# Kernel optimization log

Hardware: AMD Instinct MI355X
Metric: run time of the kernel (lower is better)

## Reference

```python
import jax, jax.numpy as jnp
import numpy as np

P = 8  # patch size (hardcoded in unfold/fold of the original module)


def conv2d(x, w, b, groups=1):
    # x: (N,C,H,W), w: (O, C//groups, 3, 3), 'SAME' padding = padding=1 for 3x3
    y = jax.lax.conv_general_dilated(
        x, w, window_strides=(1, 1), padding='SAME',
        dimension_numbers=('NCHW', 'OIHW', 'NCHW'),
        feature_group_count=groups)
    return y + b[None, :, None, None]


def unfold8(x):
    # F.unfold(kernel=8, stride=8): (N,C,H,W) -> (N, C*64, L), channel-major then
    # kernel-row/col ordering, patches in row-major order.
    N, C, H, W = x.shape
    x = x.reshape(N, C, H // P, P, W // P, P)
    x = x.transpose(0, 1, 3, 5, 2, 4)        # N,C,ki,kj,nh,nw
    return x.reshape(N, C * P * P, (H // P) * (W // P))


def fold8(x, H, W):
    # inverse of unfold8 (non-overlapping, stride == kernel)
    N = x.shape[0]
    C = x.shape[1] // (P * P)
    x = x.reshape(N, C, P, P, H // P, W // P)
    x = x.transpose(0, 1, 4, 2, 5, 3)        # N,C,nh,ki,nw,kj
    return x.reshape(N, C, H, W)


def setup_inputs() -> dict:
    key = jax.random.key(0)
    ks = jax.random.split(key, 9)
    c = 64
    x = jax.random.normal(ks[0], (16, 7, c, 64, 64), dtype=jnp.float32)
    wq = jax.random.normal(ks[1], (c, 1, 3, 3), dtype=jnp.float32) * 0.05
    wk = jax.random.normal(ks[2], (c, 1, 3, 3), dtype=jnp.float32) * 0.05
    wv = jax.random.normal(ks[3], (c, c, 3, 3), dtype=jnp.float32) * 0.05
    wc = jax.random.normal(ks[4], (c, c, 3, 3), dtype=jnp.float32) * 0.05
    bq = jnp.zeros((c,), jnp.float32)
    bk = jnp.zeros((c,), jnp.float32)
    bv = jnp.zeros((c,), jnp.float32)
    bc = jnp.zeros((c,), jnp.float32)
    return {"x": x, "wq": wq, "bq": bq, "wk": wk, "bk": bk,
            "wv": wv, "bv": bv, "wc": wc, "bc": bc}


def reference(x, wq, bq, wk, bk, wv, bv, wc, bc):
    heads = 1
    b, t, c, h, w = x.shape
    D = P * P * c          # dim
    d = D // heads         # hidden_dim per head
    L = (h // P) * (w // P)  # num patches per frame

    xf = x.reshape(-1, c, h, w)
    q = unfold8(conv2d(xf, wq, bq, groups=c))   # depthwise conv
    k = unfold8(conv2d(xf, wk, bk, groups=c))   # depthwise conv
    v = unfold8(conv2d(xf, wv, bv))             # dense conv

    def rearr(u):
        # (b*t, D, L) -> (b, heads, d, t*L)
        return u.reshape(b, t, heads, d, L).transpose(0, 2, 3, 1, 4).reshape(b, heads, d, t * L)

    q, k, v = rearr(q), rearr(k), rearr(v)

    attn = jnp.einsum('bhds,bhdu->bhsu', q, k) * (d ** -0.5)  # (b,H,tL,tL)
    attn = jax.nn.softmax(attn, axis=-1)
    out = jnp.einsum('bhsu,bhdu->bhsd', attn, v)               # (b,H,tL,d)

    out = out.reshape(b, heads, t, L, d).transpose(0, 2, 1, 4, 3).reshape(b * t, D, L)
    feat = fold8(out, h, w)
    return conv2d(feat, wc, bc).reshape(x.shape) + x
```

## Files before the change

### kernel.cpp

```cpp
#include <hip/hip_runtime.h>
#include <hip/hip_bf16.h>


namespace {
constexpr int NFR = 112;
constexpr int T_  = 7;
constexpr int B_  = 16;
constexpr int C_  = 64;
constexpr int H_  = 64;
constexpr int W_  = 64;
constexpr int S_  = 448;
constexpr int D_  = 4096;
constexpr size_t QKV_E = (size_t)B_ * S_ * D_;
constexpr size_t ATTN_E = (size_t)B_ * S_ * S_;
}

typedef __attribute__((ext_vector_type(8))) short short8v;
typedef __attribute__((ext_vector_type(4))) float float4v;

__device__ __forceinline__ float bfu2f(unsigned short u) {
    union { unsigned int i; float f; } v; v.i = ((unsigned int)u) << 16; return v.f;
}
__device__ __forceinline__ unsigned short f2bf(float f) {
    __hip_bfloat16 h = __float2bfloat16(f);
    return *reinterpret_cast<unsigned short*>(&h);
}

__device__ __forceinline__ short8v frag_ld(const char* ldsb, int r, int kByte) {
    return *(const short8v*)(ldsb + r * 128 + (kByte ^ ((r & 7) << 4)));
}

template<int NTHR>
__device__ __forceinline__ void stage_tile(char* ldsb, const unsigned short* g,
                                           int ldg, int t) {
    #pragma unroll
    for (int i = 0; i < 1024 / NTHR; ++i) {
        int e = i * NTHR + t;
        int r = e >> 3, c8 = (e & 7) * 8;
        short8v v = *(const short8v*)(g + (size_t)r * ldg + c8);
        *(short8v*)(ldsb + r * 128 + ((c8 * 2) ^ ((r & 7) << 4))) = v;
    }
}

__device__ __forceinline__ void stage_vt(char* ldsb, const unsigned short* g, int t) {
    int d0 = (t & 15) * 8;
    int u0 = (t >> 4) * 4;
    short8v r0 = *(const short8v*)(g + (size_t)(u0 + 0) * D_ + d0);
    short8v r1 = *(const short8v*)(g + (size_t)(u0 + 1) * D_ + d0);
    short8v r2 = *(const short8v*)(g + (size_t)(u0 + 2) * D_ + d0);
    short8v r3 = *(const short8v*)(g + (size_t)(u0 + 3) * D_ + d0);
    #pragma unroll
    for (int j = 0; j < 8; ++j) {
        unsigned int lo = (unsigned short)r0[j] | (((unsigned int)(unsigned short)r1[j]) << 16);
        unsigned int hi = (unsigned short)r2[j] | (((unsigned int)(unsigned short)r3[j]) << 16);
        int d = d0 + j;
        int byte = d * 128 + (((unsigned)(u0 * 2)) ^ ((d & 7) << 4));
        *(uint2*)(ldsb + byte) = uint2{lo, hi};
    }
}

__global__ __launch_bounds__(256) void prep_w2(const float* __restrict__ wv,
                                               const float* __restrict__ wc,
                                               __hip_bfloat16* __restrict__ Wt_v,
                                               __hip_bfloat16* __restrict__ Wt_c)
{
    int t = blockIdx.x * 256 + threadIdx.x;
    if (t >= 2 * 36864) return;
    int which = t >= 36864;
    int i = t - which * 36864;
    const float* s = which ? wc : wv;
    __hip_bfloat16* d = which ? Wt_c : Wt_v;
    int r = i >> 12, co = (i >> 6) & 63, ci = i & 63;
    d[i] = __float2bfloat16(s[(co * 64 + ci) * 9 + r]);
}

__global__ __launch_bounds__(256) void conv_qk_unfold3(
    const float* __restrict__ x,
    const float* __restrict__ wq, const float* __restrict__ bq,
    const float* __restrict__ wk, const float* __restrict__ bk,
    __hip_bfloat16* __restrict__ Q, __hip_bfloat16* __restrict__ K)
{
    __shared__ float xls[8][10][67];
    int py  = blockIdx.x;
    int oc8 = blockIdx.y;
    int f   = blockIdx.z;
    int t = threadIdx.x;
    int yb = py * 8 - 1;

    for (int e = t; e < 8 * 10 * 64; e += 256) {
        int col = e & 63;
        int row = (e >> 6) % 10;
        int ch  = e / 640;
        int y = yb + row;
        float v = 0.f;
        if ((unsigned)y < (unsigned)H_)
            v = x[(((size_t)f * C_ + oc8 * 8 + ch) * H_ + y) * W_ + col];
        xls[ch][row][col + 1] = v;
    }
    for (int e = t; e < 8 * 10 * 3; e += 256) {
        int which = e % 3;
        int row = (e / 3) % 10;
        int ch  = e / 30;
        xls[ch][row][which == 0 ? 0 : 64 + which] = 0.f;
    }
    __syncthreads();

    int w = t >> 6, lane = t & 63;
    int cg = lane >> 3, ky = lane & 7;
    int c  = oc8 * 8 + cg;
    float wqr[9], wkr[9];
    #pragma unroll
    for (int i = 0; i < 9; ++i) { wqr[i] = wq[c * 9 + i]; wkr[i] = wk[c * 9 + i]; }
    float bqv = bq[c], bkv = bk[c];
    int b = f / T_, tt = f % T_;
    unsigned short* Qp = (unsigned short*)Q;
    unsigned short* Kp = (unsigned short*)K;

    #pragma unroll
    for (int pi = 0; pi < 2; ++pi) {
        int px = w + pi * 4;
        int xb = px * 8;
        float acq[8], ack[8];
        #pragma unroll
        for (int j = 0; j < 8; ++j) { acq[j] = bqv; ack[j] = bkv; }
        #pragma unroll
        for (int dy = 0; dy < 3; ++dy) {
            const float* rp = &xls[cg][ky + dy][xb];
            float r[10];
            #pragma unroll
            for (int j = 0; j < 10; ++j) r[j] = rp[j];
            float w0q = wqr[dy * 3], w1q = wqr[dy * 3 + 1], w2q = wqr[dy * 3 + 2];
            float w0k = wkr[dy * 3], w1k = wkr[dy * 3 + 1], w2k = wkr[dy * 3 + 2];
            #pragma unroll
            for (int j = 0; j < 8; ++j) {
                acq[j] += w0q * r[j] + w1q * r[j + 1] + w2q * r[j + 2];
                ack[j] += w0k * r[j] + w1k * r[j + 1] + w2k * r[j + 2];
            }
        }
        int s = tt * 64 + py * 8 + px;
        size_t off = ((size_t)b * S_ + s) * D_ + (size_t)c * 64 + ky * 8;
        unsigned short pq[8], pk[8];
        #pragma unroll
        for (int j = 0; j < 8; ++j) { pq[j] = f2bf(acq[j]); pk[j] = f2bf(ack[j]); }
        *(short8v*)(Qp + off) = *(const short8v*)pq;
        *(short8v*)(Kp + off) = *(const short8v*)pk;
    }
}

template<bool IS_V>
__global__ __launch_bounds__(512, 4) void conv_mfma5(
    const void* __restrict__ src,
    const __hip_bfloat16* __restrict__ Wt,
    const float* __restrict__ bias,
    const float* __restrict__ xin,
    void* __restrict__ dst)
{
    __shared__ char xs[6 * 66 * 128];
    __shared__ char wl[2][64 * 128];
    const int f    = blockIdx.y;
    const int band = blockIdx.x;
    const int y0   = band * 4;
    const int tid  = threadIdx.x;
    const int lane = tid & 63;
    const int w    = tid >> 6;
    const int q    = lane >> 4;
    const int l15  = lane & 15;
    const int wrow = w >> 1;
    const int wco  = w & 1;

    const unsigned short* Wg = (const unsigned short*)Wt;
    const int r0w = tid >> 3, c0w = (tid & 7) * 8;
    const int wlo = r0w * 128 + ((c0w * 2) ^ ((r0w & 7) << 4));
    const unsigned short* wgl = Wg + r0w * 64 + c0w;

    short8v w0A = *(const short8v*)(wgl);

    for (int e = tid; e < 6 * 16 * 64; e += 512) {
        int x  = e & 63;
        int cg = (e >> 6) & 15;
        int r  = e >> 10;
        int y  = y0 - 1 + r;
        unsigned short p[4];
        if ((unsigned)y < (unsigned)H_) {
            #pragma unroll
            for (int j = 0; j < 4; ++j) {
                size_t gi = (((size_t)f * C_ + cg * 4 + j) * H_ + y) * W_ + x;
                if constexpr (IS_V) p[j] = f2bf(((const float*)src)[gi]);
                else                p[j] = ((const unsigned short*)src)[gi];
            }
        } else { p[0] = p[1] = p[2] = p[3] = 0; }
        int xp = x + 1;
        int byte = (r * 66 + xp) * 128 + ((cg * 8) ^ ((xp & 7) << 4));
        *(uint2*)(xs + byte) = *(uint2*)p;
    }
    for (int e = tid; e < 6 * 16 * 2; e += 512) {
        int side = e & 1;
        int cg   = (e >> 1) & 15;
        int r    = e >> 5;
        int xp   = side ? 65 : 0;
        int byte = (r * 66 + xp) * 128 + ((cg * 8) ^ ((xp & 7) << 4));
        *(uint2*)(xs + byte) = uint2{0u, 0u};
    }
    *(short8v*)(wl[0] + wlo) = w0A;
    __syncthreads();

    float4v acc[4][2] = {};
    #pragma unroll
    for (int tap = 0; tap < 9; ++tap) {
        const int ky = tap / 3, kx = tap - ky * 3;
        short8v nwA;
        if (tap + 1 < 9) {
            nwA = *(const short8v*)(wgl + (tap + 1) * 4096);
            __builtin_amdgcn_sched_barrier(0);
        }
        const char* wb = wl[tap & 1];
        const int ri = wrow + ky;
        #pragma unroll
        for (int kc = 0; kc < 2; ++kc) {
            int kB = kc * 64 + q * 16;
            short8v bfr[2];
            #pragma unroll
            for (int nt = 0; nt < 2; ++nt)
                bfr[nt] = frag_ld(wb, wco * 32 + nt * 16 + l15, kB);
            #pragma unroll
            for (int xt = 0; xt < 4; ++xt) {
                int xp = xt * 16 + l15 + kx;
                short8v av = *(const short8v*)(xs + (ri * 66 + xp) * 128 +
                                               (kB ^ ((xp & 7) << 4)));
                #pragma unroll
                for (int nt = 0; nt < 2; ++nt)
                    acc[xt][nt] = __builtin_amdgcn_mfma_f32_16x16x32_bf16(
                        av, bfr[nt], acc[xt][nt], 0, 0, 0);
            }
        }
        if (tap + 1 < 9) {
            *(short8v*)(wl[(tap + 1) & 1] + wlo) = nwA;
        }
        __syncthreads();
    }

    float bco[2];
    #pragma unroll
    for (int nt = 0; nt < 2; ++nt) bco[nt] = bias[wco * 32 + nt * 16 + l15];
    const int bb = f / T_, tt = f % T_;
    const int R = y0 + wrow;
    #pragma unroll
    for (int xt = 0; xt < 4; ++xt) {
        #pragma unroll
        for (int nt = 0; nt < 2; ++nt) {
            int co = wco * 32 + nt * 16 + l15;
            if constexpr (IS_V) {
                int s  = tt * 64 + (R >> 3) * 8 + xt * 2 + (q >> 1);
                int d0 = co * 64 + (R & 7) * 8 + (q & 1) * 4;
                unsigned short pk[4];
                #pragma unroll
                for (int j = 0; j < 4; ++j)
                    pk[j] = f2bf(acc[xt][nt][j] + bco[nt]);
                *(uint2*)((unsigned short*)dst + ((size_t)bb * S_ + s) * D_ + d0) =
                    *(const uint2*)pk;
            } else {
                size_t o = (((size_t)f * C_ + co) * H_ + R) * W_ + xt * 16 + q * 4;
                float4 rv = *(const float4*)(xin + o);
                float4 ov;
                ov.x = acc[xt][nt][0] + bco[nt] + rv.x;
                ov.y = acc[xt][nt][1] + bco[nt] + rv.y;
                ov.z = acc[xt][nt][2] + bco[nt] + rv.z;
                ov.w = acc[xt][nt][3] + bco[nt] + rv.w;
                *(float4*)((float*)dst + o) = ov;
            }
        }
    }
}

__global__ __launch_bounds__(512, 2) void gemm_qk_mfma(
    const __hip_bfloat16* __restrict__ Qg,
    const __hip_bfloat16* __restrict__ Kg,
    float* __restrict__ ATTN)
{
    __shared__ alignas(16) char lds[32768];
    char* ldsA = lds;
    char* ldsB = lds + 16384;
    int bid = blockIdx.x;
    int lb  = (bid & 7) * 32 + (bid >> 3);
    int bb  = lb >> 4;
    int m0  = ((lb >> 2) & 3) * 128;
    int n0  = (lb & 3) * 128;
    const unsigned short* Ag = (const unsigned short*)Qg + (size_t)bb * S_ * D_ + (size_t)m0 * D_;
    const unsigned short* Bg = (const unsigned short*)Kg + (size_t)bb * S_ * D_ + (size_t)n0 * D_;
    int t = threadIdx.x;
    int w = t >> 6, l = t & 63, q = l >> 4, l15 = l & 15;
    int wm = w >> 2, wn = w & 3;
    int r0 = t >> 3, c0 = (t & 7) * 8;
    int r1 = 64 + r0;
    short8v sA0, sA1, sB0, sB1;
    sA0 = *(const short8v*)(Ag + (size_t)r0 * D_ + c0);
    sA1 = *(const short8v*)(Ag + (size_t)r1 * D_ + c0);
    sB0 = *(const short8v*)(Bg + (size_t)r0 * D_ + c0);
    sB1 = *(const short8v*)(Bg + (size_t)r1 * D_ + c0);

    float4v acc[4][2] = {};
    int swz0 = (c0 * 2) ^ ((r0 & 7) << 4);
    for (int k0 = 0; k0 < D_; k0 += 64) {
        __syncthreads();
        *(short8v*)(ldsA + r0 * 128 + swz0) = sA0;
        *(short8v*)(ldsA + r1 * 128 + swz0) = sA1;
        *(short8v*)(ldsB + r0 * 128 + swz0) = sB0;
        *(short8v*)(ldsB + r1 * 128 + swz0) = sB1;
        if (k0 + 64 < D_) {
            int kn = k0 + 64;
            sA0 = *(const short8v*)(Ag + (size_t)r0 * D_ + kn + c0);
            sA1 = *(const short8v*)(Ag + (size_t)r1 * D_ + kn + c0);
            sB0 = *(const short8v*)(Bg + (size_t)r0 * D_ + kn + c0);
            sB1 = *(const short8v*)(Bg + (size_t)r1 * D_ + kn + c0);
        }
        __syncthreads();
        #pragma unroll
        for (int kc = 0; kc < 2; ++kc) {
            int kB = kc * 64 + q * 16;
            short8v a[4], b[2];
            #pragma unroll
            for (int mt = 0; mt < 4; ++mt) a[mt] = frag_ld(ldsA, wm * 64 + mt * 16 + l15, kB);
            #pragma unroll
            for (int nt = 0; nt < 2; ++nt) b[nt] = frag_ld(ldsB, wn * 32 + nt * 16 + l15, kB);
            #pragma unroll
            for (int mt = 0; mt < 4; ++mt)
                #pragma unroll
                for (int nt = 0; nt < 2; ++nt)
                    acc[mt][nt] = __builtin_amdgcn_mfma_f32_16x16x32_bf16(
                        a[mt], b[nt], acc[mt][nt], 0, 0, 0);
        }
    }
    const float scale = 1.0f / 64.0f;
    #pragma unroll
    for (int mt = 0; mt < 4; ++mt) {
        #pragma unroll
        for (int nt = 0; nt < 2; ++nt) {
            int u = n0 + wn * 32 + nt * 16 + l15;
            #pragma unroll
            for (int j = 0; j < 4; ++j) {
                int s = m0 + wm * 64 + mt * 16 + q * 4 + j;
                if (s < S_ && u < S_)
                    ATTN[((size_t)bb * S_ + s) * S_ + u] = acc[mt][nt][j] * scale;
            }
        }
    }
}

__global__ __launch_bounds__(64) void softmax_rows(const float* __restrict__ ATTN,
                                                   unsigned short* __restrict__ P)
{
    size_t row = blockIdx.x;
    const float* p = ATTN + row * S_;
    int lane = threadIdx.x;
    float vals[7];
    float m = -1e30f;
    #pragma unroll
    for (int i = 0; i < 7; ++i) { vals[i] = p[lane + i * 64]; m = fmaxf(m, vals[i]); }
    #pragma unroll
    for (int off = 32; off; off >>= 1) m = fmaxf(m, __shfl_xor(m, off));
    float sum = 0.f;
    #pragma unroll
    for (int i = 0; i < 7; ++i) { vals[i] = __expf(vals[i] - m); sum += vals[i]; }
    #pragma unroll
    for (int off = 32; off; off >>= 1) sum += __shfl_xor(sum, off);
    float inv = 1.f / sum;
    #pragma unroll
    for (int i = 0; i < 7; ++i) P[row * S_ + lane + i * 64] = f2bf(vals[i] * inv);
}

__global__ __launch_bounds__(256, 2) void gemm_pv_mfma(
    const unsigned short* __restrict__ Pg,
    const __hip_bfloat16* __restrict__ Vg,
    __hip_bfloat16* __restrict__ FEAT)
{
    __shared__ alignas(16) char lds[32768];
    char* ldsA = lds;
    char* ldsB = lds + 16384;
    int bid = blockIdx.x;
    int lb  = (bid & 7) * 256 + (bid >> 3);
    int bb  = lb >> 7;
    int tl  = lb & 127;
    int m0  = (tl >> 5) * 128;
    int n0  = (tl & 31) * 128;
    const unsigned short* Ag = Pg + (size_t)bb * S_ * S_ + (size_t)m0 * S_;
    const unsigned short* Bg = (const unsigned short*)Vg + (size_t)bb * S_ * D_ + n0;
    int t = threadIdx.x;
    int w = t >> 6, l = t & 63, q = l >> 4, l15 = l & 15;
    int wm = w >> 1, wn = w & 1;
    float4v acc[4][4] = {};
    for (int k0 = 0; k0 < S_; k0 += 64) {
        __syncthreads();
        stage_tile<256>(ldsA, Ag + k0, S_, t);
        stage_vt(ldsB, Bg + (size_t)k0 * D_, t);
        __syncthreads();
        #pragma unroll
        for (int kc = 0; kc < 2; ++kc) {
            int kB = kc * 64 + q * 16;
            short8v a[4], b[4];
            #pragma unroll
            for (int mt = 0; mt < 4; ++mt) a[mt] = frag_ld(ldsA, wm * 64 + mt * 16 + l15, kB);
            #pragma unroll
            for (int nt = 0; nt < 4; ++nt) b[nt] = frag_ld(ldsB, wn * 64 + nt * 16 + l15, kB);
            #pragma unroll
            for (int mt = 0; mt < 4; ++mt)
                #pragma unroll
                for (int nt = 0; nt < 4; ++nt)
                    acc[mt][nt] = __builtin_amdgcn_mfma_f32_16x16x32_bf16(
                        a[mt], b[nt], acc[mt][nt], 0, 0, 0);
        }
    }
    #pragma unroll
    for (int mt = 0; mt < 4; ++mt) {
        #pragma unroll
        for (int j = 0; j < 4; ++j) {
            int s = m0 + wm * 64 + mt * 16 + q * 4 + j;
            if (s >= S_) continue;
            int f  = bb * T_ + (s >> 6);
            int l6 = s & 63;
            #pragma unroll
            for (int nt = 0; nt < 4; ++nt) {
                int d = n0 + wn * 64 + nt * 16 + l15;
                int c = d >> 6, r = d & 63;
                int y  = ((l6 >> 3) << 3) + (r >> 3);
                int xx = ((l6 & 7) << 3) + (r & 7);
                FEAT[(((size_t)f * C_ + c) * H_ + y) * W_ + xx] =
                    __float2bfloat16(acc[mt][nt][j]);
            }
        }
    }
}

extern "C" void kernel_launch(void* const* d_in, const int* in_sizes, int n_in,
                              void* d_out, int out_size, void* d_ws, size_t ws_size,
                              hipStream_t stream)
{
    const float* x  = (const float*)d_in[0];
    const float* wq = (const float*)d_in[1];
    const float* bq = (const float*)d_in[2];
    const float* wk = (const float*)d_in[3];
    const float* bk = (const float*)d_in[4];
    const float* wv = (const float*)d_in[5];
    const float* bv = (const float*)d_in[6];
    const float* wc = (const float*)d_in[7];
    const float* bc = (const float*)d_in[8];
    float* out = (float*)d_out;

    __hip_bfloat16* Qb = (__hip_bfloat16*)d_ws;
    __hip_bfloat16* Kb = Qb + QKV_E;
    __hip_bfloat16* Vb = Kb + QKV_E;
    float* ATTN = (float*)(Vb + QKV_E);
    __hip_bfloat16* Wt_v = (__hip_bfloat16*)(ATTN + ATTN_E);
    __hip_bfloat16* Wt_c = Wt_v + 9 * 64 * 64;
    unsigned short* Pb   = (unsigned short*)Kb;
    __hip_bfloat16* FEAT = Qb;

    prep_w2<<<288, 256, 0, stream>>>(wv, wc, Wt_v, Wt_c);

    conv_qk_unfold3<<<dim3(8, 8, NFR), 256, 0, stream>>>(x, wq, bq, wk, bk, Qb, Kb);
    conv_mfma5<true><<<dim3(16, NFR), 512, 0, stream>>>(x, Wt_v, bv, nullptr, Vb);
    gemm_qk_mfma<<<256, 512, 0, stream>>>(Qb, Kb, ATTN);
    softmax_rows<<<B_ * S_, 64, 0, stream>>>(ATTN, Pb);
    gemm_pv_mfma<<<2048, 256, 0, stream>>>(Pb, Vb, FEAT);
    conv_mfma5<false><<<dim3(16, NFR), 512, 0, stream>>>(FEAT, Wt_c, bc, x, out);
}
```

Before: 368.7 us.

## Fuse depthwise Q/K conv into V conv kernel reusing staged LDS input

Removes the separate depthwise Q/K conv+unfold kernel and computes Q and K in an epilogue of the V conv MFMA kernel. It reuses the bf16 input tile already staged in shared memory, and loads the depthwise weights and biases into shared memory. This avoids a second full read of x from global memory and one kernel launch. In exchange, Q/K are computed from bf16-rounded inputs instead of fp32, and the V kernel gets extra LDS use and register pressure.

Result: faster. 337.2 us (-8.5%).

```diff
diff --git a/kernel.cpp b/kernel.cpp
--- a/kernel.cpp
+++ b/kernel.cpp
@@ -74,89 +74,20 @@
     d[i] = __float2bfloat16(s[(co * 64 + ci) * 9 + r]);
 }
 
-__global__ __launch_bounds__(256) void conv_qk_unfold3(
-    const float* __restrict__ x,
-    const float* __restrict__ wq, const float* __restrict__ bq,
-    const float* __restrict__ wk, const float* __restrict__ bk,
-    __hip_bfloat16* __restrict__ Q, __hip_bfloat16* __restrict__ K)
-{
-    __shared__ float xls[8][10][67];
-    int py  = blockIdx.x;
-    int oc8 = blockIdx.y;
-    int f   = blockIdx.z;
-    int t = threadIdx.x;
-    int yb = py * 8 - 1;
-
-    for (int e = t; e < 8 * 10 * 64; e += 256) {
-        int col = e & 63;
-        int row = (e >> 6) % 10;
-        int ch  = e / 640;
-        int y = yb + row;
-        float v = 0.f;
-        if ((unsigned)y < (unsigned)H_)
-            v = x[(((size_t)f * C_ + oc8 * 8 + ch) * H_ + y) * W_ + col];
-        xls[ch][row][col + 1] = v;
-    }
-    for (int e = t; e < 8 * 10 * 3; e += 256) {
-        int which = e % 3;
-        int row = (e / 3) % 10;
-        int ch  = e / 30;
-        xls[ch][row][which == 0 ? 0 : 64 + which] = 0.f;
-    }
-    __syncthreads();
-
-    int w = t >> 6, lane = t & 63;
-    int cg = lane >> 3, ky = lane & 7;
-    int c  = oc8 * 8 + cg;
-    float wqr[9], wkr[9];
-    #pragma unroll
-    for (int i = 0; i < 9; ++i) { wqr[i] = wq[c * 9 + i]; wkr[i] = wk[c * 9 + i]; }
-    float bqv = bq[c], bkv = bk[c];
-    int b = f / T_, tt = f % T_;
-    unsigned short* Qp = (unsigned short*)Q;
-    unsigned short* Kp = (unsigned short*)K;
-
-    #pragma unroll
-    for (int pi = 0; pi < 2; ++pi) {
-        int px = w + pi * 4;
-        int xb = px * 8;
-        float acq[8], ack[8];
-        #pragma unroll
-        for (int j = 0; j < 8; ++j) { acq[j] = bqv; ack[j] = bkv; }
-        #pragma unroll
-        for (int dy = 0; dy < 3; ++dy) {
-            const float* rp = &xls[cg][ky + dy][xb];
-            float r[10];
-            #pragma unroll
-            for (int j = 0; j < 10; ++j) r[j] = rp[j];
-            float w0q = wqr[dy * 3], w1q = wqr[dy * 3 + 1], w2q = wqr[dy * 3 + 2];
-            float w0k = wkr[dy * 3], w1k = wkr[dy * 3 + 1], w2k = wkr[dy * 3 + 2];
-            #pragma unroll
-            for (int j = 0; j < 8; ++j) {
-                acq[j] += w0q * r[j] + w1q * r[j + 1] + w2q * r[j + 2];
-                ack[j] += w0k * r[j] + w1k * r[j + 1] + w2k * r[j + 2];
-            }
-        }
-        int s = tt * 64 + py * 8 + px;
-        size_t off = ((size_t)b * S_ + s) * D_ + (size_t)c * 64 + ky * 8;
-        unsigned short pq[8], pk[8];
-        #pragma unroll
-        for (int j = 0; j < 8; ++j) { pq[j] = f2bf(acq[j]); pk[j] = f2bf(ack[j]); }
-        *(short8v*)(Qp + off) = *(const short8v*)pq;
-        *(short8v*)(Kp + off) = *(const short8v*)pk;
-    }
-}
-
 template<bool IS_V>
-__global__ __launch_bounds__(512, 4) void conv_mfma5(
+__global__ __launch_bounds__(512, 4) void conv_mfma6(
     const void* __restrict__ src,
     const __hip_bfloat16* __restrict__ Wt,
     const float* __restrict__ bias,
     const float* __restrict__ xin,
-    void* __restrict__ dst)
+    void* __restrict__ dst,
+    const float* __restrict__ wq, const float* __restrict__ bq,
+    const float* __restrict__ wk, const float* __restrict__ bk,
+    unsigned short* __restrict__ Qout, unsigned short* __restrict__ Kout)
 {
     __shared__ char xs[6 * 66 * 128];
     __shared__ char wl[2][64 * 128];
+    __shared__ float wqk_s[IS_V ? 1280 : 1];
     const int f    = blockIdx.y;
     const int band = blockIdx.x;
     const int y0   = band * 4;
@@ -174,6 +105,17 @@
     const unsigned short* wgl = Wg + r0w * 64 + c0w;
 
     short8v w0A = *(const short8v*)(wgl);
+
+    if constexpr (IS_V) {
+        for (int e = tid; e < 1280; e += 512) {
+            float v;
+            if (e < 576)       v = wq[e];
+            else if (e < 1152) v = wk[e - 576];
+            else if (e < 1216) v = bq[e - 1152];
+            else               v = bk[e - 1216];
+            wqk_s[e] = v;
+        }
+    }
 
     for (int e = tid; e < 6 * 16 * 64; e += 512) {
         int x  = e & 63;
@@ -267,6 +209,66 @@
                 ov.z = acc[xt][nt][2] + bco[nt] + rv.z;
                 ov.w = acc[xt][nt][3] + bco[nt] + rv.w;
                 *(float4*)((float*)dst + o) = ov;
+            }
+        }
+    }
+
+    if constexpr (IS_V) {
+        const int cg8  = lane >> 3;
+        const int half = (lane >> 2) & 1;
+        const int r2   = lane & 3;
+        const int px   = w;
+        const int yk   = ((band & 1) << 2) + r2;
+        const int s    = tt * 64 + (band >> 1) * 8 + px;
+        #pragma unroll
+        for (int p = 0; p < 2; ++p) {
+            const int c0 = cg8 * 8 + half * 4 + p * 2;
+            float acq[2][8], ack[2][8];
+            float bq0 = wqk_s[1152 + c0], bq1 = wqk_s[1152 + c0 + 1];
+            float bk0 = wqk_s[1216 + c0], bk1 = wqk_s[1216 + c0 + 1];
+            #pragma unroll
+            for (int j = 0; j < 8; ++j) {
+                acq[0][j] = bq0; acq[1][j] = bq1;
+                ack[0][j] = bk0; ack[1][j] = bk1;
+            }
+            #pragma unroll
+            for (int dy = 0; dy < 3; ++dy) {
+                const int ri = r2 + dy;
+                float rv0[10], rv1[10];
+                #pragma unroll
+                for (int u = 0; u < 10; ++u) {
+                    int xp = px * 8 + u;
+                    int byte = (ri * 66 + xp) * 128 + ((c0 * 2) ^ ((xp & 7) << 4));
+                    unsigned int pr = *(const unsigned int*)(xs + byte);
+                    rv0[u] = bfu2f((unsigned short)(pr & 0xffffu));
+                    rv1[u] = bfu2f((unsigned short)(pr >> 16));
+                }
+                #pragma unroll
+                for (int kx = 0; kx < 3; ++kx) {
+                    float wq0 = wqk_s[c0 * 9 + dy * 3 + kx];
+                    float wq1 = wqk_s[(c0 + 1) * 9 + dy * 3 + kx];
+                    float wk0 = wqk_s[576 + c0 * 9 + dy * 3 + kx];
+                    float wk1 = wqk_s[576 + (c0 + 1) * 9 + dy * 3 + kx];
+                    #pragma unroll
+                    for (int j = 0; j < 8; ++j) {
+                        acq[0][j] += wq0 * rv0[j + kx];
+                        acq[1][j] += wq1 * rv1[j + kx];
+                        ack[0][j] += wk0 * rv0[j + kx];
+                        ack[1][j] += wk1 * rv1[j + kx];
+                    }
+                }
+            }
+            #pragma unroll
+            for (int i = 0; i < 2; ++i) {
+                unsigned short pq[8], pk[8];
+                #pragma unroll
+                for (int j = 0; j < 8; ++j) {
+                    pq[j] = f2bf(acq[i][j]);
+                    pk[j] = f2bf(ack[i][j]);
+                }
+                size_t off = ((size_t)bb * S_ + s) * D_ + (size_t)(c0 + i) * 64 + yk * 8;
+                *(short8v*)(Qout + off) = *(const short8v*)pq;
+                *(short8v*)(Kout + off) = *(const short8v*)pk;
             }
         }
     }
@@ -456,10 +458,13 @@
 
     prep_w2<<<288, 256, 0, stream>>>(wv, wc, Wt_v, Wt_c);
 
-    conv_qk_unfold3<<<dim3(8, 8, NFR), 256, 0, stream>>>(x, wq, bq, wk, bk, Qb, Kb);
-    conv_mfma5<true><<<dim3(16, NFR), 512, 0, stream>>>(x, Wt_v, bv, nullptr, Vb);
+    conv_mfma6<true><<<dim3(16, NFR), 512, 0, stream>>>(
+        x, Wt_v, bv, nullptr, Vb,
+        wq, bq, wk, bk, (unsigned short*)Qb, (unsigned short*)Kb);
     gemm_qk_mfma<<<256, 512, 0, stream>>>(Qb, Kb, ATTN);
     softmax_rows<<<B_ * S_, 64, 0, stream>>>(ATTN, Pb);
     gemm_pv_mfma<<<2048, 256, 0, stream>>>(Pb, Vb, FEAT);
-    conv_mfma5<false><<<dim3(16, NFR), 512, 0, stream>>>(FEAT, Wt_c, bc, x, out);
-}
+    conv_mfma6<false><<<dim3(16, NFR), 512, 0, stream>>>(
+        FEAT, Wt_c, bc, x, out,
+        nullptr, nullptr, nullptr, nullptr, nullptr, nullptr);
+}
```
